# Kernel tuning notes

Hardware: AMD Instinct MI355X
Metric: run time of the kernel (lower is better)

Reference implementation:

```python
import jax, jax.numpy as jnp
import numpy as np

B, C_IN, H, W = 4, 512, 188, 188
SHARED_CH = 64
NUM_CLASS = 3
M = 200
NUM_MAX = 500
STRIDE = 8
PCR = (-75.2, -75.2, -2.0, 75.2, 75.2, 4.0)
VOX = (0.1, 0.1, 0.15)
OUT_CH = (2, 1, 3, 2, 1, 3)  # center, center_z, dim, rot, iou, hm
MIN_RADIUS = 2.0
OVERLAP = 0.1
INIT_BIAS = -2.19


def conv3x3(x, w):
    return jax.lax.conv_general_dilated(x, w, (1, 1), 'SAME',
                                        dimension_numbers=('NCHW', 'OIHW', 'NCHW'))


def bn_relu(x, p):
    # p: [4, C] = gamma, beta, running_mean, running_var (inference-mode BN)
    g, b, m, v = p[0], p[1], p[2], p[3]
    scale = (g * jax.lax.rsqrt(v + 1e-5))[None, :, None, None]
    y = (x - m[None, :, None, None]) * scale + b[None, :, None, None]
    return jax.nn.relu(y)


def gaussian_radius(height, width, min_overlap):
    # Faithful to OpenPCDet centernet_utils.gaussian_radius
    b1 = height + width
    c1 = width * height * (1 - min_overlap) / (1 + min_overlap)
    sq1 = jnp.sqrt(jnp.maximum(b1 * b1 - 4.0 * c1, 0.0))
    r1 = (b1 + sq1) / 2.0
    b2 = 2.0 * (height + width)
    c2 = (1 - min_overlap) * width * height
    sq2 = jnp.sqrt(jnp.maximum(b2 * b2 - 16.0 * c2, 0.0))
    r2 = (b2 + sq2) / 2.0
    a3 = 4.0 * min_overlap
    b3 = -2.0 * min_overlap * (height + width)
    c3 = (min_overlap - 1.0) * width * height
    sq3 = jnp.sqrt(jnp.maximum(b3 * b3 - 4.0 * a3 * c3, 0.0))
    r3 = (b3 + sq3) / 2.0
    return jnp.minimum(jnp.minimum(r1, r2), r3)


def assign_targets(gt_boxes):
    # gt_boxes: [B, M, 8] = x, y, z, dx, dy, dz, heading, class(1..NUM_CLASS)
    x, y, z = gt_boxes[..., 0], gt_boxes[..., 1], gt_boxes[..., 2]
    dx, dy, dz = gt_boxes[..., 3], gt_boxes[..., 4], gt_boxes[..., 5]
    heading = gt_boxes[..., 6]
    cls = jax.lax.stop_gradient(gt_boxes[..., 7]).astype(jnp.int32)

    cx = jnp.clip((x - PCR[0]) / VOX[0] / STRIDE, 0.0, W - 0.5)  # [B,M]
    cy = jnp.clip((y - PCR[1]) / VOX[1] / STRIDE, 0.0, H - 0.5)
    cxi = jax.lax.stop_gradient(jnp.floor(cx)).astype(jnp.int32)  # .int() trunc == floor (>=0)
    cyi = jax.lax.stop_gradient(jnp.floor(cy)).astype(jnp.int32)

    dxp = dx / VOX[0] / STRIDE
    dyp = dy / VOX[1] / STRIDE
    r = gaussian_radius(dxp, dyp, OVERLAP)
    r = jnp.maximum(jnp.floor(jax.lax.stop_gradient(r)), MIN_RADIUS)  # clamp_min(r.int(), 2)
    sigma = (2.0 * r + 1.0) / 6.0
    valid = (dx > 0) & (dy > 0)  # [B,M]

    ox = jnp.arange(W, dtype=jnp.int32)[None, None, :] - cxi[..., None]  # [B,M,W]
    oy = jnp.arange(H, dtype=jnp.int32)[None, None, :] - cyi[..., None]  # [B,M,H]
    d2 = (oy.astype(jnp.float32) ** 2)[:, :, :, None] + (ox.astype(jnp.float32) ** 2)[:, :, None, :]
    g = jnp.exp(-d2 / (2.0 * sigma * sigma)[:, :, None, None])  # [B,M,H,W]
    win = (jnp.abs(oy)[:, :, :, None] <= r[:, :, None, None]) & \
          (jnp.abs(ox)[:, :, None, :] <= r[:, :, None, None])
    g = jnp.where(win & valid[:, :, None, None], g, 0.0)

    # per-class max-splat (draw_gaussian_to_heatmap uses torch.max overlap)
    heatmap = jnp.stack(
        [jnp.max(jnp.where((cls == c + 1)[:, :, None, None], g, 0.0), axis=1)
         for c in range(NUM_CLASS)], axis=1)  # [B,NUM_CLASS,H,W]

    vf = valid.astype(gt_boxes.dtype)
    vals = jnp.stack([cx - cxi.astype(cx.dtype), cy - cyi.astype(cy.dtype), z,
                      jnp.log(dx), jnp.log(dy), jnp.log(dz),
                      jnp.cos(heading), jnp.sin(heading)], axis=-1) * vf[..., None]
    target_boxes = jnp.zeros((B, NUM_MAX, 8), gt_boxes.dtype).at[:, :M].set(vals)
    ind_vals = (cyi * W + cxi) * valid.astype(jnp.int32)
    inds = jnp.zeros((B, NUM_MAX), jnp.int32).at[:, :M].set(ind_vals)
    mask = jnp.zeros((B, NUM_MAX), jnp.int32).at[:, :M].set(valid.astype(jnp.int32))
    return heatmap, target_boxes, inds, mask


def setup_inputs() -> dict:
    key = jax.random.key(0)
    ks = jax.random.split(key, 16)
    spatial_features = jax.random.normal(ks[0], (B, C_IN, H, W), jnp.float32)
    x = jax.random.uniform(ks[1], (B, M), minval=-70.0, maxval=70.0)
    y = jax.random.uniform(ks[2], (B, M), minval=-70.0, maxval=70.0)
    z = jax.random.uniform(ks[3], (B, M), minval=-1.0, maxval=1.0)
    dx = jax.random.uniform(ks[4], (B, M), minval=1.5, maxval=5.0)
    dy = jax.random.uniform(ks[5], (B, M), minval=1.5, maxval=5.0)
    dz = jax.random.uniform(ks[6], (B, M), minval=1.0, maxval=3.0)
    hd = jax.random.uniform(ks[7], (B, M), minval=-np.pi, maxval=np.pi)
    cls = jax.random.randint(ks[8], (B, M), 1, NUM_CLASS + 1).astype(jnp.float32)
    gt_boxes = jnp.stack([x, y, z, dx, dy, dz, hd, cls], axis=-1)

    def mk_bn(k, lead):
        kk = jax.random.split(k, 4)
        g = 1.0 + 0.1 * jax.random.normal(kk[0], lead + (SHARED_CH,))
        b = 0.1 * jax.random.normal(kk[1], lead + (SHARED_CH,))
        m = 0.1 * jax.random.normal(kk[2], lead + (SHARED_CH,))
        v = jax.random.uniform(kk[3], lead + (SHARED_CH,), minval=0.5, maxval=1.5)
        return jnp.stack([g, b, m, v], axis=len(lead))

    w_shared = jax.random.normal(ks[9], (SHARED_CH, C_IN, 3, 3)) * (1.0 / np.sqrt(C_IN * 9))
    bn_shared = mk_bn(ks[10], ())
    w1_heads = jax.random.normal(ks[11], (6, SHARED_CH, SHARED_CH, 3, 3)) * (1.0 / np.sqrt(SHARED_CH * 9))
    bn_heads = mk_bn(ks[12], (6,))
    w2_heads = jax.random.normal(ks[13], (6, 3, SHARED_CH, 3, 3)) * (1.0 / np.sqrt(SHARED_CH * 9))
    b2_heads = jnp.zeros((6, 3), jnp.float32).at[5].set(INIT_BIAS)  # hm branch bias = -2.19
    return {'spatial_features': spatial_features, 'gt_boxes': gt_boxes,
            'w_shared': w_shared, 'bn_shared': bn_shared,
            'w1_heads': w1_heads, 'bn_heads': bn_heads,
            'w2_heads': w2_heads, 'b2_heads': b2_heads}


def reference(spatial_features, gt_boxes, w_shared, bn_shared,
              w1_heads, bn_heads, w2_heads, b2_heads):
    shared = bn_relu(conv3x3(spatial_features, w_shared), bn_shared)  # [B,64,H,W]

    def branch(w1, bnp, w2, b2):
        h = bn_relu(conv3x3(shared, w1), bnp)
        return conv3x3(h, w2) + b2[None, :, None, None]  # [B,3,H,W] (out padded to 3)

    outs = jax.vmap(branch)(w1_heads, bn_heads, w2_heads, b2_heads)  # [6,B,3,H,W]
    head_out = jnp.concatenate([outs[i, :, :OUT_CH[i]] for i in range(6)], axis=1)  # [B,12,H,W]

    heatmap, target_boxes, inds, mask = assign_targets(gt_boxes)
    return head_out, heatmap, target_boxes, inds, mask
```

## Files before the change

### kernel.cpp

```cpp
#include <hip/hip_runtime.h>
#include <hip/hip_bf16.h>

#define HWD 188
#define NPX (HWD*HWD)
#define NB 4
#define CIN 512
#define CH 64
#define MBOX 200
#define NMAX 500

#define HEAD_SZ (NB*12*NPX)
#define HM_OFF  HEAD_SZ
#define TB_OFF  (HM_OFF + NB*3*NPX)
#define IND_OFF (TB_OFF + NB*NMAX*8)
#define MSK_OFF (IND_OFF + NB*NMAX)

typedef short sh8 __attribute__((ext_vector_type(8)));
typedef float f4 __attribute__((ext_vector_type(4)));
typedef unsigned short us4 __attribute__((ext_vector_type(4)));

__device__ __constant__ int d_cum[6]  = {0, 2, 3, 6, 8, 9};
__device__ __constant__ int d_outc[6] = {2, 1, 3, 2, 1, 3};

__device__ __forceinline__ unsigned short bf16_bits(float v) {
  union { __hip_bfloat16 h; unsigned short u; } cv;
  cv.h = __float2bfloat16(v);
  return cv.u;
}

__device__ __forceinline__ int xcd_swz(int bid, int grid) {
  return (bid & 7) * (grid >> 3) + (bid >> 3);
}

__global__ __launch_bounds__(256) void wprep(
    const float* __restrict__ ws_, const float* __restrict__ w1_,
    const float* __restrict__ w2_, unsigned short* __restrict__ w1b,
    unsigned short* __restrict__ w2b, unsigned short* __restrict__ w3b) {
  int e = blockIdx.x * 256 + threadIdx.x;
  const int N1 = 9 * 16 * 64 * 32;
  const int N2 = 6 * 9 * 64 * 64;
  const int N3 = 6 * 9 * 16 * 64;
  if (e < N1) {
    int icr = e & 31; int r1 = e >> 5;
    int oc = r1 & 63; int r2 = r1 >> 6;
    int icq = r2 & 15; int tap = r2 >> 4;
    w1b[e] = bf16_bits(ws_[(oc * 512 + icq * 32 + icr) * 9 + tap]);
  } else if (e < N1 + N2) {
    int f = e - N1;
    int h = f / (9 * 64 * 64); int r = f % (9 * 64 * 64);
    int tap = r / (64 * 64); int r2 = r % (64 * 64);
    int oc = r2 / 64; int ic = r2 % 64;
    w2b[f] = bf16_bits(w1_[((h * 64 + oc) * 64 + ic) * 9 + tap]);
  } else if (e < N1 + N2 + N3) {
    int f = e - N1 - N2;
    int h = f / (9 * 16 * 64); int r = f % (9 * 16 * 64);
    int tap = r / (16 * 64); int r2 = r % (16 * 64);
    int oc = r2 / 64; int ic = r2 % 64;
    float v = (oc < 3) ? w2_[((h * 3 + oc) * 64 + ic) * 9 + tap] : 0.f;
    w3b[f] = bf16_bits(v);
  }
}

#define C1_PXS 40
#define C1_LDS (10*18*C1_PXS)
__global__ __launch_bounds__(256, 4) void conv1_mfma(
    const float* __restrict__ sf,
    const unsigned short* __restrict__ wb,
    const float* __restrict__ bnp,
    unsigned short* __restrict__ outp) {
  __shared__ __align__(16) short s_in[2][C1_LDS];
  const int t = threadIdx.x;
  const int swz = xcd_swz(blockIdx.x, 1152);
  const int b = swz / 288;
  const int tt = swz % 288;
  const int y0 = (tt / 12) * 8, x0 = (tt % 12) * 16;
  const int w = t >> 6, lane = t & 63, ln = lane & 15, kg = lane >> 4;
  const int rg = w & 1, og = w >> 1;

  const bool st_act = (t < 240);
  const int icg = t & 3, cg = (t >> 2) % 6, sr = (t >> 2) / 6;
  const int gy_s = y0 - 1 + sr;
  const int gx0_s = x0 - 4 + cg * 4;
  const bool row_ok = (gy_s >= 0 && gy_s < HWD);
  const bool vec_ok = (gx0_s >= 0 && gx0_s + 3 < HWD);
  const float* sbase = sf + (((long long)b * CIN + icg * 8) * HWD + gy_s) * HWD + gx0_s;

  f4 acc[2][4];
#pragma unroll
  for (int i = 0; i < 2; ++i)
#pragma unroll
    for (int j = 0; j < 4; ++j) acc[i][j] = (f4){0.f, 0.f, 0.f, 0.f};

  f4 st[8];
#pragma unroll
  for (int j = 0; j < 8; ++j) st[j] = (f4){0.f, 0.f, 0.f, 0.f};

#define C1_LOAD(IC0)                                                        \
  do {                                                                      \
    if (st_act && row_ok) {                                                 \
      const float* p = sbase + (long long)(IC0) * NPX;                      \
      if (vec_ok) {                                                         \
        _Pragma("unroll")                                                   \
        for (int j = 0; j < 8; ++j)                                         \
          st[j] = *reinterpret_cast<const f4*>(p + (long long)j * NPX);     \
      } else {                                                              \
        _Pragma("unroll")                                                   \
        for (int j = 0; j < 8; ++j) st[j] = (f4){0.f, 0.f, 0.f, 0.f};       \
        _Pragma("unroll")                                                   \
        for (int k = 0; k < 4; ++k) {                                       \
          int gx = gx0_s + k;                                               \
          if (gx >= 0 && gx < HWD) {                                        \
            _Pragma("unroll")                                               \
            for (int j = 0; j < 8; ++j) st[j][k] = p[(long long)j * NPX + k];\
          }                                                                 \
        }                                                                   \
      }                                                                     \
    } else {                                                                \
      _Pragma("unroll")                                                     \
      for (int j = 0; j < 8; ++j) st[j] = (f4){0.f, 0.f, 0.f, 0.f};         \
    }                                                                       \
  } while (0)

#define C1_WRITE(BUF)                                                       \
  do {                                                                      \
    if (st_act) {                                                           \
      _Pragma("unroll")                                                     \
      for (int k = 0; k < 4; ++k) {                                         \
        int col = cg * 4 + k - 3;                                           \
        if ((unsigned)col < 18u) {                                          \
          sh8 pk;                                                           \
          _Pragma("unroll")                                                 \
          for (int j = 0; j < 8; ++j) pk[j] = (short)bf16_bits(st[j][k]);   \
          *reinterpret_cast<sh8*>(&(BUF)[(sr * 18 + col) * C1_PXS + icg * 8]) = pk; \
        }                                                                   \
      }                                                                     \
    }                                                                       \
  } while (0)

  C1_LOAD(0);
  C1_WRITE(s_in[0]);
  __syncthreads();

  for (int s = 0; s < 16; ++s) {
    const short* cur = s_in[s & 1];
    if (s < 15) C1_LOAD((s + 1) * 32);
    __builtin_amdgcn_s_setprio(1);
#pragma unroll
    for (int tap = 0; tap < 9; ++tap) {
      const int ky = tap / 3, kx = tap % 3;
      sh8 af[2];
#pragma unroll
      for (int i = 0; i < 2; ++i)
        af[i] = *reinterpret_cast<const sh8*>(
            wb + (((tap * 16 + s) * 64) + (2 * og + i) * 16 + ln) * 32 + kg * 8);
#pragma unroll
      for (int nt = 0; nt < 4; ++nt) {
        const int rr = 4 * rg + nt + ky;
        const int cc = ln + kx;
        sh8 bf = *reinterpret_cast<const sh8*>(&cur[(rr * 18 + cc) * C1_PXS + kg * 8]);
#pragma unroll
        for (int i = 0; i < 2; ++i)
          acc[i][nt] = __builtin_amdgcn_mfma_f32_16x16x32_bf16(
              af[i], bf, acc[i][nt], 0, 0, 0);
      }
    }
    __builtin_amdgcn_s_setprio(0);
    if (s < 15) C1_WRITE(s_in[(s & 1) ^ 1]);
    __syncthreads();
  }

#pragma unroll
  for (int i = 0; i < 2; ++i) {
    const int ocb = (2 * og + i) * 16 + kg * 4;
    f4 g4 = *reinterpret_cast<const f4*>(bnp + ocb);
    f4 b4 = *reinterpret_cast<const f4*>(bnp + 64 + ocb);
    f4 m4 = *reinterpret_cast<const f4*>(bnp + 128 + ocb);
    f4 v4 = *reinterpret_cast<const f4*>(bnp + 192 + ocb);
    f4 sc, bi;
#pragma unroll
    for (int j = 0; j < 4; ++j) {
      sc[j] = g4[j] * rsqrtf(v4[j] + 1e-5f);
      bi[j] = b4[j] - m4[j] * sc[j];
    }
#pragma unroll
    for (int nt = 0; nt < 4; ++nt) {
      int y = y0 + 4 * rg + nt;
      int x = x0 + ln;
      if (y < HWD && x < HWD) {
        us4 pk;
#pragma unroll
        for (int j = 0; j < 4; ++j)
          pk[j] = bf16_bits(fmaxf(acc[i][nt][j] * sc[j] + bi[j], 0.f));
        *reinterpret_cast<us4*>(outp + (((long long)b * HWD + y) * HWD + x) * 64 + ocb) = pk;
      }
    }
  }
#undef C1_LOAD
#undef C1_WRITE
}

__global__ __launch_bounds__(512, 2) void conv23_fused(
    const unsigned short* __restrict__ inp,
    const unsigned short* __restrict__ w2b,
    const unsigned short* __restrict__ w3b,
    const float* __restrict__ bnH,
    const float* __restrict__ b2,
    float* __restrict__ hout) {
  __shared__ __align__(16) short s_in[240 * 64];
  __shared__ __align__(16) short s_buf[180 * 64];
  const int t = threadIdx.x;
  const int swz = xcd_swz(blockIdx.x, 6912);
  const int h = swz % 6;
  const int tile = swz / 6;
  const int b = tile / 288;
  const int tt = tile % 288;
  const int y0 = (tt / 12) * 8, x0 = (tt % 12) * 16;
  const int w = t >> 6, lane = t & 63, ln = lane & 15, kg = lane >> 4;
  const int og = w & 1, pg = w >> 1;

#pragma unroll
  for (int k = 0; k < 4; ++k) {
    int idx = t + k * 512;
    if (idx < 1920) {
      int g = idx & 7, px = idx >> 3;
      int r = px / 20, c = px - r * 20;
      int gy = y0 - 2 + r, gx = x0 - 2 + c;
      sh8 v = (sh8){0, 0, 0, 0, 0, 0, 0, 0};
      if (gy >= 0 && gy < HWD && gx >= 0 && gx < HWD)
        v = *reinterpret_cast<const sh8*>(
            &inp[(((long long)b * HWD + gy) * HWD + gx) * 64 + g * 8]);
      *reinterpret_cast<sh8*>(&s_in[px * 64 + ((g ^ (px & 7)) * 8)]) = v;
    }
  }

  int base_in[3], qpx[3];
  bool wr_ok[3], img_ok[3];
#pragma unroll
  for (int nt = 0; nt < 3; ++nt) {
    int q = (pg * 3 + nt) * 16 + ln;
    wr_ok[nt] = (q < 180);
    if (q > 179) q = 179;
    int r2 = q / 18, c2 = q - (q / 18) * 18;
    base_in[nt] = r2 * 20 + c2;
    qpx[nt] = q;
    int gy2 = y0 - 1 + r2, gx2 = x0 - 1 + c2;
    img_ok[nt] = (gy2 >= 0 && gy2 < HWD && gx2 >= 0 && gx2 < HWD);
  }
  __syncthreads();

  f4 acc2[3][2];
#pragma unroll
  for (int k = 0; k < 3; ++k)
#pragma unroll
    for (int mt = 0; mt < 2; ++mt) acc2[k][mt] = (f4){0.f, 0.f, 0.f, 0.f};

#pragma unroll
  for (int icq = 0; icq < 2; ++icq) {
    const int gread = icq * 4 + kg;
    __builtin_amdgcn_s_setprio(1);
#pragma unroll
    for (int tap = 0; tap < 9; ++tap) {
      const int toff = (tap / 3) * 20 + (tap % 3);
      sh8 af0 = *reinterpret_cast<const sh8*>(
          w2b + (((h * 9 + tap) * 64) + og * 32 + ln) * 64 + icq * 32 + kg * 8);
      sh8 af1 = *reinterpret_cast<const sh8*>(
          w2b + (((h * 9 + tap) * 64) + og * 32 + 16 + ln) * 64 + icq * 32 + kg * 8);
#pragma unroll
      for (int nt = 0; nt < 3; ++nt) {
        const int pin = base_in[nt] + toff;
        sh8 bf = *reinterpret_cast<const sh8*>(
            &s_in[pin * 64 + ((gread ^ (pin & 7)) * 8)]);
        acc2[nt][0] = __builtin_amdgcn_mfma_f32_16x16x32_bf16(af0, bf, acc2[nt][0], 0, 0, 0);
        acc2[nt][1] = __builtin_amdgcn_mfma_f32_16x16x32_bf16(af1, bf, acc2[nt][1], 0, 0, 0);
      }
    }
    __builtin_amdgcn_s_setprio(0);
  }

  const float* bnp = bnH + h * 256;
#pragma unroll
  for (int mt = 0; mt < 2; ++mt) {
    const int cch = og * 32 + mt * 16 + kg * 4;
    f4 g4 = *reinterpret_cast<const f4*>(bnp + cch);
    f4 b4 = *reinterpret_cast<const f4*>(bnp + 64 + cch);
    f4 m4 = *reinterpret_cast<const f4*>(bnp + 128 + cch);
    f4 v4 = *reinterpret_cast<const f4*>(bnp + 192 + cch);
    f4 sc, bi;
#pragma unroll
    for (int j = 0; j < 4; ++j) {
      sc[j] = g4[j] * rsqrtf(v4[j] + 1e-5f);
      bi[j] = b4[j] - m4[j] * sc[j];
    }
    const int g8 = cch >> 3;
    const int soff = (kg & 1) * 4;
#pragma unroll
    for (int nt = 0; nt < 3; ++nt) {
      if (wr_ok[nt]) {
        us4 pk = {0, 0, 0, 0};
        if (img_ok[nt]) {
#pragma unroll
          for (int j = 0; j < 4; ++j)
            pk[j] = bf16_bits(fmaxf(acc2[nt][mt][j] * sc[j] + bi[j], 0.f));
        }
        *reinterpret_cast<us4*>(
            &s_buf[qpx[nt] * 64 + ((g8 ^ (qpx[nt] & 7)) * 8) + soff]) = pk;
      }
    }
  }
  __syncthreads();

  f4 acc3 = (f4){0.f, 0.f, 0.f, 0.f};
  __builtin_amdgcn_s_setprio(1);
#pragma unroll
  for (int kq = 0; kq < 2; ++kq) {
#pragma unroll
    for (int tap = 0; tap < 9; ++tap) {
      const int toff3 = (tap / 3 - 1) * 18 + (tap % 3 - 1);
      sh8 af3 = *reinterpret_cast<const sh8*>(
          w3b + (((h * 9 + tap) * 16) + ln) * 64 + kq * 32 + kg * 8);
      const int q3 = (w + 1) * 18 + (ln + 1) + toff3;
      const int g = kq * 4 + kg;
      sh8 bf3 = *reinterpret_cast<const sh8*>(
          &s_buf[q3 * 64 + ((g ^ (q3 & 7)) * 8)]);
      acc3 = __builtin_amdgcn_mfma_f32_16x16x32_bf16(af3, bf3, acc3, 0, 0, 0);
    }
  }
  __builtin_amdgcn_s_setprio(0);

  const int c_off = d_cum[h], noc = d_outc[h];
  const int yy = y0 + w, xx = x0 + ln;
  if (yy < HWD && xx < HWD) {
#pragma unroll
    for (int j = 0; j < 4; ++j) {
      int oc = kg * 4 + j;
      if (oc < noc)
        hout[((long long)b * 12 + c_off + oc) * NPX + yy * HWD + xx] =
            acc3[j] + b2[h * 3 + oc];
    }
  }
}

__global__ __launch_bounds__(256) void targets_kernel(
    const float* __restrict__ gt, float* __restrict__ out, float* __restrict__ boxp) {
  int idx = blockIdx.x * 256 + threadIdx.x;
  if (idx >= NB * NMAX) return;
  int b = idx / NMAX, j = idx - b * NMAX;
  float vals[8] = {0, 0, 0, 0, 0, 0, 0, 0};
  float indf = 0.f, mkf = 0.f;
  if (j < MBOX) {
    const float* g = gt + (b * MBOX + j) * 8;
    float x = g[0], y = g[1], z = g[2], dx = g[3], dy = g[4], dz = g[5];
    float hd = g[6], cls = g[7];
    float cx = (x - (-75.2f)) / 0.1f / 8.0f;
    cx = fminf(fmaxf(cx, 0.0f), (float)HWD - 0.5f);
    float cy = (y - (-75.2f)) / 0.1f / 8.0f;
    cy = fminf(fmaxf(cy, 0.0f), (float)HWD - 0.5f);
    float cxf = floorf(cx), cyf = floorf(cy);
    int cxi = (int)cxf, cyi = (int)cyf;
    float hh = dx / 0.1f / 8.0f;
    float ww = dy / 0.1f / 8.0f;
    const float ov = 0.1f;
    float b1 = hh + ww;
    float c1 = ww * hh * (1.0f - ov) / (1.0f + ov);
    float sq1 = sqrtf(fmaxf(b1 * b1 - 4.0f * c1, 0.0f));
    float r1 = (b1 + sq1) / 2.0f;
    float b2_ = 2.0f * (hh + ww);
    float c2 = (1.0f - ov) * ww * hh;
    float sq2 = sqrtf(fmaxf(b2_ * b2_ - 16.0f * c2, 0.0f));
    float r2 = (b2_ + sq2) / 2.0f;
    float a3 = 4.0f * ov;
    float b3 = -2.0f * ov * (hh + ww);
    float c3 = (ov - 1.0f) * ww * hh;
    float sq3 = sqrtf(fmaxf(b3 * b3 - 4.0f * a3 * c3, 0.0f));
    float r3 = (b3 + sq3) / 2.0f;
    float r = fminf(fminf(r1, r2), r3);
    r = fmaxf(floorf(r), 2.0f);
    float sigma = (2.0f * r + 1.0f) / 6.0f;
    float inv2s2 = 1.0f / (2.0f * sigma * sigma);
    bool valid = (dx > 0.0f) && (dy > 0.0f);
    float vf = valid ? 1.0f : 0.0f;
    vals[0] = (cx - cxf) * vf;
    vals[1] = (cy - cyf) * vf;
    vals[2] = z * vf;
    vals[3] = logf(dx) * vf;
    vals[4] = logf(dy) * vf;
    vals[5] = logf(dz) * vf;
    vals[6] = cosf(hd) * vf;
    vals[7] = sinf(hd) * vf;
    indf = (float)((cyi * HWD + cxi) * (valid ? 1 : 0));
    mkf = vf;
    float* bp = boxp + (b * MBOX + j) * 8;
    bp[0] = cxf; bp[1] = cyf; bp[2] = r; bp[3] = inv2s2;
    bp[4] = valid ? cls : 0.0f; bp[5] = 0.f; bp[6] = 0.f; bp[7] = 0.f;
  }
  float* tb = out + TB_OFF + (b * NMAX + j) * 8;
#pragma unroll
  for (int k = 0; k < 8; ++k) tb[k] = vals[k];
  out[IND_OFF + b * NMAX + j] = indf;
  out[MSK_OFF + b * NMAX + j] = mkf;
}

__global__ __launch_bounds__(256) void heatmap_kernel(
    const float* __restrict__ boxp, float* __restrict__ out) {
  __shared__ float s_bp[MBOX][5];
  const int t = threadIdx.x, b = blockIdx.y;
  for (int e = t; e < MBOX * 5; e += 256) {
    int j = e / 5, k = e - j * 5;
    s_bp[j][k] = boxp[(b * MBOX + j) * 8 + k];
  }
  __syncthreads();
  int p = blockIdx.x * 256 + t;
  if (p >= NPX) return;
  int y = p / HWD, x = p - y * HWD;
  float a0 = 0.f, a1 = 0.f, a2 = 0.f;
  for (int j = 0; j < MBOX; ++j) {
    int c = (int)s_bp[j][4];
    if (c == 0) continue;
    float ox = (float)x - s_bp[j][0];
    float oy = (float)y - s_bp[j][1];
    float r = s_bp[j][2];
    if (fabsf(ox) <= r && fabsf(oy) <= r) {
      float gg = expf(-(ox * ox + oy * oy) * s_bp[j][3]);
      if (c == 1) a0 = fmaxf(a0, gg);
      else if (c == 2) a1 = fmaxf(a1, gg);
      else a2 = fmaxf(a2, gg);
    }
  }
  int base = HM_OFF + (b * 3 * HWD + y) * HWD + x;
  out[base] = a0;
  out[base + NPX] = a1;
  out[base + 2 * NPX] = a2;
}

extern "C" void kernel_launch(void* const* d_in, const int* in_sizes, int n_in,
                              void* d_out, int out_size, void* d_ws, size_t ws_size,
                              hipStream_t stream) {
  (void)in_sizes; (void)n_in; (void)out_size; (void)ws_size;
  const float* sf = (const float*)d_in[0];
  const float* gt = (const float*)d_in[1];
  const float* w_shared = (const float*)d_in[2];
  const float* bn_shared = (const float*)d_in[3];
  const float* w1 = (const float*)d_in[4];
  const float* bnH = (const float*)d_in[5];
  const float* w2 = (const float*)d_in[6];
  const float* b2 = (const float*)d_in[7];
  float* out = (float*)d_out;
  char* ws = (char*)d_ws;

  const size_t SH = (size_t)NB * NPX * 64 * 2;
  unsigned short* shared_t = (unsigned short*)ws;
  unsigned short* w1b = (unsigned short*)(ws + SH);
  unsigned short* w2b = (unsigned short*)(ws + SH + 589824);
  unsigned short* w3b = (unsigned short*)(ws + SH + 589824 + 442368);
  float* boxp = (float*)(ws + SH + 589824 + 442368 + 110592);

  wprep<<<2232, 256, 0, stream>>>(w_shared, w1, w2, w1b, w2b, w3b);

  conv1_mfma<<<1152, 256, 0, stream>>>(sf, w1b, bn_shared, shared_t);

  conv23_fused<<<6912, 512, 0, stream>>>(shared_t, w2b, w3b, bnH, b2, out);

  targets_kernel<<<(NB * NMAX + 255) / 256, 256, 0, stream>>>(gt, out, boxp);
  heatmap_kernel<<<dim3((NPX + 255) / 256, NB), 256, 0, stream>>>(boxp, out);
}
```

Baseline: 640.1 us.

## Drop LDS input staging in conv23 and read halo directly from global

The fused second/third conv kernel no longer stages the input halo tile into shared memory. Each wave instead loads its B-fragments straight from global memory with per-tap bounds checks. The block shrinks from 512 to 256 threads, and each wave now covers all 64 output channels and two output rows. This removes the LDS fill and one barrier and frees shared memory for higher occupancy. In exchange the overlapping 3x3 halo is refetched from global/L2 nine times, and register pressure grows with the larger accumulator set.

```diff
diff --git a/kernel.cpp b/kernel.cpp
--- a/kernel.cpp
+++ b/kernel.cpp
@@ -199,14 +199,13 @@
 #undef C1_WRITE
 }
 
-__global__ __launch_bounds__(512, 2) void conv23_fused(
+__global__ __launch_bounds__(256, 4) void conv23_fused(
     const unsigned short* __restrict__ inp,
     const unsigned short* __restrict__ w2b,
     const unsigned short* __restrict__ w3b,
     const float* __restrict__ bnH,
     const float* __restrict__ b2,
     float* __restrict__ hout) {
-  __shared__ __align__(16) short s_in[240 * 64];
   __shared__ __align__(16) short s_buf[180 * 64];
   const int t = threadIdx.x;
   const int swz = xcd_swz(blockIdx.x, 6912);
@@ -216,71 +215,57 @@
   const int tt = tile % 288;
   const int y0 = (tt / 12) * 8, x0 = (tt % 12) * 16;
   const int w = t >> 6, lane = t & 63, ln = lane & 15, kg = lane >> 4;
-  const int og = w & 1, pg = w >> 1;
-
-#pragma unroll
-  for (int k = 0; k < 4; ++k) {
-    int idx = t + k * 512;
-    if (idx < 1920) {
-      int g = idx & 7, px = idx >> 3;
-      int r = px / 20, c = px - r * 20;
-      int gy = y0 - 2 + r, gx = x0 - 2 + c;
-      sh8 v = (sh8){0, 0, 0, 0, 0, 0, 0, 0};
-      if (gy >= 0 && gy < HWD && gx >= 0 && gx < HWD)
-        v = *reinterpret_cast<const sh8*>(
-            &inp[(((long long)b * HWD + gy) * HWD + gx) * 64 + g * 8]);
-      *reinterpret_cast<sh8*>(&s_in[px * 64 + ((g ^ (px & 7)) * 8)]) = v;
-    }
-  }
-
-  int base_in[3], qpx[3];
-  bool wr_ok[3], img_ok[3];
+
+  const unsigned short* pbase[3];
+  int iy0[3], ix0[3], qpx[3];
+  bool wr_ok[3];
 #pragma unroll
   for (int nt = 0; nt < 3; ++nt) {
-    int q = (pg * 3 + nt) * 16 + ln;
+    int q = (w * 3 + nt) * 16 + ln;
     wr_ok[nt] = (q < 180);
     if (q > 179) q = 179;
+    qpx[nt] = q;
     int r2 = q / 18, c2 = q - (q / 18) * 18;
-    base_in[nt] = r2 * 20 + c2;
-    qpx[nt] = q;
-    int gy2 = y0 - 1 + r2, gx2 = x0 - 1 + c2;
-    img_ok[nt] = (gy2 >= 0 && gy2 < HWD && gx2 >= 0 && gx2 < HWD);
-  }
-  __syncthreads();
-
-  f4 acc2[3][2];
-#pragma unroll
-  for (int k = 0; k < 3; ++k)
-#pragma unroll
-    for (int mt = 0; mt < 2; ++mt) acc2[k][mt] = (f4){0.f, 0.f, 0.f, 0.f};
+    iy0[nt] = y0 - 2 + r2;
+    ix0[nt] = x0 - 2 + c2;
+    pbase[nt] = inp + (((long long)b * HWD + iy0[nt]) * HWD + ix0[nt]) * 64;
+  }
+
+  f4 acc2[3][4];
+#pragma unroll
+  for (int nt = 0; nt < 3; ++nt)
+#pragma unroll
+    for (int mt = 0; mt < 4; ++mt) acc2[nt][mt] = (f4){0.f, 0.f, 0.f, 0.f};
 
 #pragma unroll
   for (int icq = 0; icq < 2; ++icq) {
-    const int gread = icq * 4 + kg;
-    __builtin_amdgcn_s_setprio(1);
 #pragma unroll
     for (int tap = 0; tap < 9; ++tap) {
-      const int toff = (tap / 3) * 20 + (tap % 3);
-      sh8 af0 = *reinterpret_cast<const sh8*>(
-          w2b + (((h * 9 + tap) * 64) + og * 32 + ln) * 64 + icq * 32 + kg * 8);
-      sh8 af1 = *reinterpret_cast<const sh8*>(
-          w2b + (((h * 9 + tap) * 64) + og * 32 + 16 + ln) * 64 + icq * 32 + kg * 8);
+      const int ky = tap / 3, kx = tap % 3;
+      sh8 af[4];
+#pragma unroll
+      for (int mt = 0; mt < 4; ++mt)
+        af[mt] = *reinterpret_cast<const sh8*>(
+            w2b + (((h * 9 + tap) * 64) + mt * 16 + ln) * 64 + icq * 32 + kg * 8);
 #pragma unroll
       for (int nt = 0; nt < 3; ++nt) {
-        const int pin = base_in[nt] + toff;
-        sh8 bf = *reinterpret_cast<const sh8*>(
-            &s_in[pin * 64 + ((gread ^ (pin & 7)) * 8)]);
-        acc2[nt][0] = __builtin_amdgcn_mfma_f32_16x16x32_bf16(af0, bf, acc2[nt][0], 0, 0, 0);
-        acc2[nt][1] = __builtin_amdgcn_mfma_f32_16x16x32_bf16(af1, bf, acc2[nt][1], 0, 0, 0);
-      }
-    }
-    __builtin_amdgcn_s_setprio(0);
+        sh8 bf = (sh8){0, 0, 0, 0, 0, 0, 0, 0};
+        if ((unsigned)(iy0[nt] + ky) < (unsigned)HWD &&
+            (unsigned)(ix0[nt] + kx) < (unsigned)HWD)
+          bf = *reinterpret_cast<const sh8*>(
+              pbase[nt] + (ky * HWD + kx) * 64 + icq * 32 + kg * 8);
+#pragma unroll
+        for (int mt = 0; mt < 4; ++mt)
+          acc2[nt][mt] = __builtin_amdgcn_mfma_f32_16x16x32_bf16(
+              af[mt], bf, acc2[nt][mt], 0, 0, 0);
+      }
+    }
   }
 
   const float* bnp = bnH + h * 256;
 #pragma unroll
-  for (int mt = 0; mt < 2; ++mt) {
-    const int cch = og * 32 + mt * 16 + kg * 4;
+  for (int mt = 0; mt < 4; ++mt) {
+    const int cch = mt * 16 + kg * 4;
     f4 g4 = *reinterpret_cast<const f4*>(bnp + cch);
     f4 b4 = *reinterpret_cast<const f4*>(bnp + 64 + cch);
     f4 m4 = *reinterpret_cast<const f4*>(bnp + 128 + cch);
@@ -297,7 +282,8 @@
     for (int nt = 0; nt < 3; ++nt) {
       if (wr_ok[nt]) {
         us4 pk = {0, 0, 0, 0};
-        if (img_ok[nt]) {
+        if ((unsigned)(iy0[nt] + 1) < (unsigned)HWD &&
+            (unsigned)(ix0[nt] + 1) < (unsigned)HWD) {
 #pragma unroll
           for (int j = 0; j < 4; ++j)
             pk[j] = bf16_bits(fmaxf(acc2[nt][mt][j] * sc[j] + bi[j], 0.f));
@@ -309,7 +295,9 @@
   }
   __syncthreads();
 
-  f4 acc3 = (f4){0.f, 0.f, 0.f, 0.f};
+  f4 acc3[2];
+#pragma unroll
+  for (int i = 0; i < 2; ++i) acc3[i] = (f4){0.f, 0.f, 0.f, 0.f};
   __builtin_amdgcn_s_setprio(1);
 #pragma unroll
   for (int kq = 0; kq < 2; ++kq) {
@@ -318,24 +306,30 @@
       const int toff3 = (tap / 3 - 1) * 18 + (tap % 3 - 1);
       sh8 af3 = *reinterpret_cast<const sh8*>(
           w3b + (((h * 9 + tap) * 16) + ln) * 64 + kq * 32 + kg * 8);
-      const int q3 = (w + 1) * 18 + (ln + 1) + toff3;
       const int g = kq * 4 + kg;
-      sh8 bf3 = *reinterpret_cast<const sh8*>(
-          &s_buf[q3 * 64 + ((g ^ (q3 & 7)) * 8)]);
-      acc3 = __builtin_amdgcn_mfma_f32_16x16x32_bf16(af3, bf3, acc3, 0, 0, 0);
+#pragma unroll
+      for (int i = 0; i < 2; ++i) {
+        const int q3 = (w * 2 + i + 1) * 18 + (ln + 1) + toff3;
+        sh8 bf3 = *reinterpret_cast<const sh8*>(
+            &s_buf[q3 * 64 + ((g ^ (q3 & 7)) * 8)]);
+        acc3[i] = __builtin_amdgcn_mfma_f32_16x16x32_bf16(af3, bf3, acc3[i], 0, 0, 0);
+      }
     }
   }
   __builtin_amdgcn_s_setprio(0);
 
   const int c_off = d_cum[h], noc = d_outc[h];
-  const int yy = y0 + w, xx = x0 + ln;
-  if (yy < HWD && xx < HWD) {
-#pragma unroll
-    for (int j = 0; j < 4; ++j) {
-      int oc = kg * 4 + j;
-      if (oc < noc)
-        hout[((long long)b * 12 + c_off + oc) * NPX + yy * HWD + xx] =
-            acc3[j] + b2[h * 3 + oc];
+#pragma unroll
+  for (int i = 0; i < 2; ++i) {
+    const int yy = y0 + w * 2 + i, xx = x0 + ln;
+    if (yy < HWD && xx < HWD) {
+#pragma unroll
+      for (int j = 0; j < 4; ++j) {
+        int oc = kg * 4 + j;
+        if (oc < noc)
+          hout[((long long)b * 12 + c_off + oc) * NPX + yy * HWD + xx] =
+              acc3[i][j] + b2[h * 3 + oc];
+      }
     }
   }
 }
@@ -458,7 +452,7 @@
 
   conv1_mfma<<<1152, 256, 0, stream>>>(sf, w1b, bn_shared, shared_t);
 
-  conv23_fused<<<6912, 512, 0, stream>>>(shared_t, w2b, w3b, bnH, b2, out);
+  conv23_fused<<<6912, 256, 0, stream>>>(shared_t, w2b, w3b, bnH, b2, out);
 
   targets_kernel<<<(NB * NMAX + 255) / 256, 256, 0, stream>>>(gt, out, boxp);
   heatmap_kernel<<<dim3((NPX + 255) / 256, NB), 256, 0, stream>>>(boxp, out);
```

Measured after the change: 821.8 us. 28.4% more time.
